# Kernel tuning notes

Measured on AMD Instinct MI355X. Metric: run time of the kernel, lower is better.

The kernel has to match this reference:

```python
import jax, jax.numpy as jnp
import numpy as np

N, M, D = 2048, 100000, 128
K = 5


def setup_inputs() -> dict:
    key = jax.random.key(0)
    k1, k2 = jax.random.split(key)
    features = jax.random.normal(k1, (N, D), dtype=jnp.float32)
    memory_bank = jax.random.normal(k2, (M, D), dtype=jnp.float32)
    # normalization buffers computed during fit(); use plausible scalars
    min_val = jnp.zeros((), dtype=jnp.float32)
    max_val = jnp.ones((), dtype=jnp.float32)
    return {
        "features": features,
        "memory_bank": memory_bank,
        "min_val": min_val,
        "max_val": max_val,
        "n_neighbors": K,
    }


def reference(features, memory_bank, min_val, max_val, n_neighbors):
    x2 = jnp.sum(features * features, axis=1, keepdims=True)        # (N,1)
    y2 = jnp.sum(memory_bank * memory_bank, axis=1)[None, :]        # (1,M)
    d2 = x2 + y2 - 2.0 * (features @ memory_bank.T)                 # (N,M)
    dist = jnp.sqrt(jnp.maximum(d2, 0.0))
    # k smallest distances per query (topk largest=False)
    neg_knn, _ = jax.lax.top_k(-dist, n_neighbors)                  # (N,K)
    knn = -neg_knn
    # min-max normalization with fitted stats
    knn = (knn - min_val) / (max_val - min_val)
    return knn.mean(axis=1)                                         # (N,)
```

## Files before the change

### kernel.cpp

```cpp
#include <hip/hip_runtime.h>
#include <stdint.h>

#define N_Q 2048
#define M_B 100000
#define D_DIM 128
#define KNN 5
#define SLABS_TOTAL 1563
#define M_PAD (SLABS_TOTAL * 64)
#define CHUNKS 64
#define SPC 25
#define CLS 16
#define FTOT (CHUNKS * CLS)
#define ROWBLOCKS 16
#define TROWS 128
#define BIGF 3.0e38f
#define NEGF -3.0e38f


typedef __attribute__((ext_vector_type(8))) short short8;
typedef __attribute__((ext_vector_type(4))) unsigned short ushort4v;
typedef __attribute__((ext_vector_type(8))) unsigned short ushort8v;
typedef __attribute__((ext_vector_type(4))) float f32x4;

static __device__ __forceinline__ unsigned short f2bf(float f) {
  unsigned int u = __builtin_bit_cast(unsigned int, f);
  u = (u + 0x7FFFu + ((u >> 16) & 1u)) >> 16;
  return (unsigned short)u;
}

static __device__ __forceinline__ void gload_lds16(const void* g, void* l) {
  __builtin_amdgcn_global_load_lds((const __attribute__((address_space(1))) unsigned int*)g,
                                   (__attribute__((address_space(3))) unsigned int*)l, 16, 0, 0);
}
static __device__ __forceinline__ void gload_lds4(const void* g, void* l) {
  __builtin_amdgcn_global_load_lds((const __attribute__((address_space(1))) unsigned int*)g,
                                   (__attribute__((address_space(3))) unsigned int*)l, 4, 0, 0);
}

#define DPPADD(v, ctrl)                                                              \
  do {                                                                               \
    int _t = __builtin_amdgcn_update_dpp(0, __builtin_bit_cast(int, (v)), (ctrl),    \
                                         0xf, 0xf, false);                           \
    (v) = (v) + __builtin_bit_cast(float, _t);                                       \
  } while (0)

__global__ __launch_bounds__(256) void k_prep(const float* __restrict__ Y,
                                              unsigned short* __restrict__ ybf,
                                              float* __restrict__ ny2) {
  const int s = blockIdx.x;
  const int t = threadIdx.x;
  __shared__ __align__(16) unsigned short tile[8192];
  __shared__ float redy[64 * 33];
#pragma unroll
  for (int i = 0; i < 8; ++i) {
    const int u = i * 256 + t;
    const int rowl = u >> 5;
    const int q = u & 31;
    const int rowg = s * 64 + rowl;
    const int rowc = (rowg < M_B) ? rowg : (M_B - 1);
    const float4 v = ((const float4*)Y)[(size_t)rowc * 32 + q];
    redy[rowl * 33 + q] = v.x * v.x + v.y * v.y + v.z * v.z + v.w * v.w;
    ushort4v o;
    o[0] = f2bf(v.x); o[1] = f2bf(v.y); o[2] = f2bf(v.z); o[3] = f2bf(v.w);
    *(ushort4v*)(tile + (size_t)(((q >> 1) * 64 + rowl) * 8 + (q & 1) * 4)) = o;
  }
  __syncthreads();
  {
    const int rowl = t >> 2;
    const int k = t & 3;
    float ss = 0.f;
#pragma unroll
    for (int j = 0; j < 8; ++j) ss += redy[rowl * 33 + k * 8 + j];
    DPPADD(ss, 0xB1);
    DPPADD(ss, 0x4E);
    const int rowg = s * 64 + rowl;
    if ((t & 3) == 0) ny2[(size_t)s * 64 + rowl] = (rowg < M_B) ? (-0.5f * ss) : NEGF;
  }
#pragma unroll
  for (int i = 0; i < 4; ++i) {
    const int u = i * 256 + t;
    *(ushort8v*)(ybf + ((size_t)s * 1024 + u) * 8) = *(const ushort8v*)(tile + u * 8);
  }
}

__global__ __launch_bounds__(256, 4) void k_main(const float* __restrict__ X,
                                                 const unsigned short* __restrict__ ybf,
                                                 const float* __restrict__ ny2,
                                                 float* __restrict__ rsm) {
  __shared__ __align__(16) char smem[39168];
  unsigned short* ys = (unsigned short*)smem;
  float* ny2s = (float*)(smem + 32768);

  const int bid = blockIdx.x;
  const int chunk = bid % CHUNKS;
  const int rowblock = bid / CHUNKS;
  const int row0 = rowblock * TROWS;

  const int cs0 = chunk * SPC;
  int nslab = SLABS_TOTAL - cs0;
  if (nslab > SPC) nslab = SPC;
  if (nslab < 0) nslab = 0;

  const int t = threadIdx.x;
  const int wave = t >> 6;
  const int lane = t & 63;
  const int lm = lane & 15;
  const int lq = lane >> 4;

  short8 afrag[2][4];
#pragma unroll
  for (int rt = 0; rt < 2; ++rt)
#pragma unroll
    for (int ks = 0; ks < 4; ++ks) {
      const float* xr = X + (size_t)(row0 + wave * 32 + rt * 16 + lm) * D_DIM + ks * 32 + lq * 8;
      const float4 a = *(const float4*)xr;
      const float4 b = *(const float4*)(xr + 4);
      short8 f;
      f[0] = (short)f2bf(a.x); f[1] = (short)f2bf(a.y);
      f[2] = (short)f2bf(a.z); f[3] = (short)f2bf(a.w);
      f[4] = (short)f2bf(b.x); f[5] = (short)f2bf(b.y);
      f[6] = (short)f2bf(b.z); f[7] = (short)f2bf(b.w);
      afrag[rt][ks] = f;
    }

  for (int j = wave; j < nslab; j += 4)
    gload_lds4(ny2 + (size_t)(cs0 + j) * 64 + lane, ny2s + (size_t)j * 64);
  __syncthreads();

  float prmax[2][4];
#pragma unroll
  for (int rt = 0; rt < 2; ++rt)
#pragma unroll
    for (int rr = 0; rr < 4; ++rr) prmax[rt][rr] = NEGF;

  if (nslab > 0) {
    const unsigned short* src = ybf + (size_t)cs0 * 8192;
#pragma unroll
    for (int i = 0; i < 4; ++i) {
      const int ub = i * 256 + wave * 64;
      gload_lds16(src + (size_t)(ub + lane) * 8, ys + (size_t)ub * 8);
    }
  }

  for (int s = 0; s < nslab; ++s) {
    unsigned short* yb = ys + (size_t)(s & 1) * 8192;
    if (s + 1 < nslab) {
      const unsigned short* src = ybf + (size_t)(cs0 + s + 1) * 8192;
      unsigned short* dst = ys + (size_t)((s + 1) & 1) * 8192;
#pragma unroll
      for (int i = 0; i < 4; ++i) {
        const int ub = i * 256 + wave * 64;
        gload_lds16(src + (size_t)(ub + lane) * 8, dst + (size_t)ub * 8);
      }
      asm volatile("s_waitcnt vmcnt(4)" ::: "memory");
    } else {
      asm volatile("s_waitcnt vmcnt(0)" ::: "memory");
    }
    __builtin_amdgcn_s_barrier();

    float y2c[4];
#pragma unroll
    for (int ct = 0; ct < 4; ++ct) y2c[ct] = ny2s[s * 64 + ct * 16 + lm];

    f32x4 acc[2][4];
#pragma unroll
    for (int rt = 0; rt < 2; ++rt)
#pragma unroll
      for (int ct = 0; ct < 4; ++ct)
#pragma unroll
        for (int rr = 0; rr < 4; ++rr) acc[rt][ct][rr] = y2c[ct];

    __builtin_amdgcn_s_setprio(1);
#pragma unroll
    for (int ct = 0; ct < 4; ++ct) {
      short8 bfr[4];
#pragma unroll
      for (int ks = 0; ks < 4; ++ks)
        bfr[ks] = *(const short8*)(yb + (size_t)(((ks * 4 + lq) * 64 + ct * 16 + lm)) * 8);
#pragma unroll
      for (int rt = 0; rt < 2; ++rt)
#pragma unroll
        for (int ks = 0; ks < 4; ++ks)
          acc[rt][ct] = __builtin_amdgcn_mfma_f32_16x16x32_bf16(afrag[rt][ks], bfr[ks],
                                                                acc[rt][ct], 0, 0, 0);
    }
    __builtin_amdgcn_s_setprio(0);

#pragma unroll
    for (int rt = 0; rt < 2; ++rt)
#pragma unroll
      for (int rr = 0; rr < 4; ++rr) {
        const float cm = fmaxf(fmaxf(fmaxf(acc[rt][0][rr], acc[rt][1][rr]),
                                     acc[rt][2][rr]), acc[rt][3][rr]);
        prmax[rt][rr] = fmaxf(prmax[rt][rr], cm);
      }

    __builtin_amdgcn_s_barrier();
  }

#pragma unroll
  for (int rt = 0; rt < 2; ++rt)
#pragma unroll
    for (int rr = 0; rr < 4; ++rr) {
      const int lrow = wave * 32 + rt * 16 + lq * 4 + rr;
      rsm[(size_t)(row0 + lrow) * FTOT + chunk * CLS + lm] = prmax[rt][rr];
    }
}

__global__ __launch_bounds__(256) void k_scan(const float* __restrict__ rsm,
                                              const float* __restrict__ X,
                                              const float* __restrict__ minp,
                                              const float* __restrict__ maxp,
                                              float* __restrict__ out) {
  const int wave = threadIdx.x >> 6;
  const int lane = threadIdx.x & 63;
  const int row = blockIdx.x * 4 + wave;
  const float* rp = rsm + (size_t)row * FTOT;

  float x2;
  {
    const float a = X[(size_t)row * D_DIM + lane];
    const float b = X[(size_t)row * D_DIM + 64 + lane];
    x2 = a * a + b * b;
#pragma unroll
    for (int off = 1; off < 64; off <<= 1) x2 += __shfl_xor(x2, off);
  }

  float t0 = NEGF, t1 = NEGF, t2 = NEGF, t3 = NEGF, t4 = NEGF;
  for (int i = lane; i < FTOT; i += 64) {
    const float v = rp[i];
    if (v > t4) {
      float m = v;
      float n3 = fminf(t3, m); m = fmaxf(t3, m);
      float n2 = fminf(t2, m); m = fmaxf(t2, m);
      float n1 = fminf(t1, m); m = fmaxf(t1, m);
      float n0 = fminf(t0, m); m = fmaxf(t0, m);
      t0 = m; t1 = n0; t2 = n1; t3 = n2; t4 = n3;
    }
  }

  int k = 0;
  float sum = 0.f;
#pragma unroll
  for (int r = 0; r < KNN; ++r) {
    float head = (k == 0) ? t0 : (k == 1) ? t1 : (k == 2) ? t2 : (k == 3) ? t3
               : (k == 4) ? t4 : NEGF;
    float m = head;
#pragma unroll
    for (int off = 1; off < 64; off <<= 1) m = fmaxf(m, __shfl_xor(m, off));
    const unsigned long long mask = __ballot(head == m);
    const int first = __ffsll(mask) - 1;
    if (lane == first) ++k;
    sum += sqrtf(fmaxf(x2 - 2.f * m, 0.f));
  }
  if (lane == 0) {
    const float mn = minp[0], mx = maxp[0];
    out[row] = (sum * (1.0f / KNN) - mn) / (mx - mn);
  }
}

extern "C" void kernel_launch(void* const* d_in, const int* in_sizes, int n_in,
                              void* d_out, int out_size, void* d_ws, size_t ws_size,
                              hipStream_t stream) {
  const float* X = (const float*)d_in[0];
  const float* Y = (const float*)d_in[1];
  const float* minp = (const float*)d_in[2];
  const float* maxp = (const float*)d_in[3];
  float* out = (float*)d_out;

  char* ws = (char*)d_ws;
  size_t off = 0;
  unsigned short* ybf = (unsigned short*)(ws + off); off += (size_t)M_PAD * D_DIM * 2;
  float* ny2 = (float*)(ws + off);                   off += (size_t)M_PAD * 4;
  float* rsm = (float*)(ws + off);                   off += (size_t)N_Q * FTOT * 4;

  k_prep<<<dim3(SLABS_TOTAL), dim3(256), 0, stream>>>(Y, ybf, ny2);
  k_main<<<dim3(ROWBLOCKS * CHUNKS), dim3(256), 0, stream>>>(X, ybf, ny2, rsm);
  k_scan<<<dim3(N_Q / 4), dim3(256), 0, stream>>>(rsm, X, minp, maxp, out);
}
```

Baseline: 146.7 us.

## Switch main GEMM to 32x32x16 MFMA with 256-row tiles per block

Replaces the 16x16x32 bf16 MFMA tiling with 32x32x16 MFMA and doubles rows per block from 128 to 256, so each wave covers 64 query rows. The LDS layout of the memory-bank slab is read with a new per-lane offset, and per-row maxima are merged across lane halves with a shuffle before being written. The aim is to reuse each B fragment across more rows, halving how often the bank is streamed from global memory, and to lower MFMA issue overhead. In exchange it uses more registers (occupancy hint drops from 4 to 2 blocks per CU), launches half as many blocks, and removes the setprio hints.

```diff
diff --git a/kernel.cpp b/kernel.cpp
--- a/kernel.cpp
+++ b/kernel.cpp
@@ -11,8 +11,8 @@
 #define SPC 25
 #define CLS 16
 #define FTOT (CHUNKS * CLS)
-#define ROWBLOCKS 16
-#define TROWS 128
+#define ROWBLOCKS 8
+#define TROWS 256
 #define BIGF 3.0e38f
 #define NEGF -3.0e38f
 
@@ -20,7 +20,7 @@
 typedef __attribute__((ext_vector_type(8))) short short8;
 typedef __attribute__((ext_vector_type(4))) unsigned short ushort4v;
 typedef __attribute__((ext_vector_type(8))) unsigned short ushort8v;
-typedef __attribute__((ext_vector_type(4))) float f32x4;
+typedef __attribute__((ext_vector_type(16))) float f32x16;
 
 static __device__ __forceinline__ unsigned short f2bf(float f) {
   unsigned int u = __builtin_bit_cast(unsigned int, f);
@@ -83,7 +83,7 @@
   }
 }
 
-__global__ __launch_bounds__(256, 4) void k_main(const float* __restrict__ X,
+__global__ __launch_bounds__(256, 2) void k_main(const float* __restrict__ X,
                                                  const unsigned short* __restrict__ ybf,
                                                  const float* __restrict__ ny2,
                                                  float* __restrict__ rsm) {
@@ -104,15 +104,15 @@
   const int t = threadIdx.x;
   const int wave = t >> 6;
   const int lane = t & 63;
-  const int lm = lane & 15;
-  const int lq = lane >> 4;
-
-  short8 afrag[2][4];
+  const int l31 = lane & 31;
+  const int lq5 = lane >> 5;
+
+  short8 afrag[2][8];
 #pragma unroll
   for (int rt = 0; rt < 2; ++rt)
 #pragma unroll
-    for (int ks = 0; ks < 4; ++ks) {
-      const float* xr = X + (size_t)(row0 + wave * 32 + rt * 16 + lm) * D_DIM + ks * 32 + lq * 8;
+    for (int ks = 0; ks < 8; ++ks) {
+      const float* xr = X + (size_t)(row0 + wave * 64 + rt * 32 + l31) * D_DIM + ks * 16 + lq5 * 8;
       const float4 a = *(const float4*)xr;
       const float4 b = *(const float4*)(xr + 4);
       short8 f;
@@ -127,11 +127,13 @@
     gload_lds4(ny2 + (size_t)(cs0 + j) * 64 + lane, ny2s + (size_t)j * 64);
   __syncthreads();
 
-  float prmax[2][4];
+  float prmax[2][16];
 #pragma unroll
   for (int rt = 0; rt < 2; ++rt)
 #pragma unroll
-    for (int rr = 0; rr < 4; ++rr) prmax[rt][rr] = NEGF;
+    for (int r = 0; r < 16; ++r) prmax[rt][r] = NEGF;
+
+  const int blane = lq5 * 512 + l31 * 8;
 
   if (nslab > 0) {
     const unsigned short* src = ybf + (size_t)cs0 * 8192;
@@ -143,10 +145,10 @@
   }
 
   for (int s = 0; s < nslab; ++s) {
-    unsigned short* yb = ys + (size_t)(s & 1) * 8192;
+    const unsigned short* yb = ys + (size_t)((s & 1) * 8192) + blane;
     if (s + 1 < nslab) {
       const unsigned short* src = ybf + (size_t)(cs0 + s + 1) * 8192;
-      unsigned short* dst = ys + (size_t)((s + 1) & 1) * 8192;
+      unsigned short* dst = ys + (size_t)(((s + 1) & 1) * 8192);
 #pragma unroll
       for (int i = 0; i < 4; ++i) {
         const int ub = i * 256 + wave * 64;
@@ -158,52 +160,53 @@
     }
     __builtin_amdgcn_s_barrier();
 
-    float y2c[4];
-#pragma unroll
-    for (int ct = 0; ct < 4; ++ct) y2c[ct] = ny2s[s * 64 + ct * 16 + lm];
-
-    f32x4 acc[2][4];
+    const float y2c0 = ny2s[s * 64 + l31];
+    const float y2c1 = ny2s[s * 64 + 32 + l31];
+
+    f32x16 acc[2][2];
 #pragma unroll
     for (int rt = 0; rt < 2; ++rt)
 #pragma unroll
-      for (int ct = 0; ct < 4; ++ct)
-#pragma unroll
-        for (int rr = 0; rr < 4; ++rr) acc[rt][ct][rr] = y2c[ct];
-
-    __builtin_amdgcn_s_setprio(1);
-#pragma unroll
-    for (int ct = 0; ct < 4; ++ct) {
-      short8 bfr[4];
-#pragma unroll
-      for (int ks = 0; ks < 4; ++ks)
-        bfr[ks] = *(const short8*)(yb + (size_t)(((ks * 4 + lq) * 64 + ct * 16 + lm)) * 8);
+      for (int r = 0; r < 16; ++r) {
+        acc[rt][0][r] = y2c0;
+        acc[rt][1][r] = y2c1;
+      }
+
+    short8 bfr[2][8];
+#pragma unroll
+    for (int ct = 0; ct < 2; ++ct)
+#pragma unroll
+      for (int ks = 0; ks < 8; ++ks)
+        bfr[ct][ks] = *(const short8*)(yb + ks * 1024 + ct * 256);
+
+#pragma unroll
+    for (int ct = 0; ct < 2; ++ct)
 #pragma unroll
       for (int rt = 0; rt < 2; ++rt)
 #pragma unroll
-        for (int ks = 0; ks < 4; ++ks)
-          acc[rt][ct] = __builtin_amdgcn_mfma_f32_16x16x32_bf16(afrag[rt][ks], bfr[ks],
+        for (int ks = 0; ks < 8; ++ks)
+          acc[rt][ct] = __builtin_amdgcn_mfma_f32_32x32x16_bf16(afrag[rt][ks], bfr[ct][ks],
                                                                 acc[rt][ct], 0, 0, 0);
-    }
-    __builtin_amdgcn_s_setprio(0);
 
 #pragma unroll
     for (int rt = 0; rt < 2; ++rt)
 #pragma unroll
-      for (int rr = 0; rr < 4; ++rr) {
-        const float cm = fmaxf(fmaxf(fmaxf(acc[rt][0][rr], acc[rt][1][rr]),
-                                     acc[rt][2][rr]), acc[rt][3][rr]);
-        prmax[rt][rr] = fmaxf(prmax[rt][rr], cm);
+      for (int r = 0; r < 16; ++r)
+        prmax[rt][r] = fmaxf(prmax[rt][r], fmaxf(acc[rt][0][r], acc[rt][1][r]));
+
+    __builtin_amdgcn_s_barrier();
+  }
+
+#pragma unroll
+  for (int rt = 0; rt < 2; ++rt)
+#pragma unroll
+    for (int r = 0; r < 16; ++r) {
+      float v = prmax[rt][r];
+      v = fmaxf(v, __shfl_xor(v, 16));
+      if ((lane & 16) == 0) {
+        const int lrow = wave * 64 + rt * 32 + (r & 3) + 8 * (r >> 2) + 4 * lq5;
+        rsm[(size_t)(row0 + lrow) * FTOT + chunk * CLS + (lane & 15)] = v;
       }
-
-    __builtin_amdgcn_s_barrier();
-  }
-
-#pragma unroll
-  for (int rt = 0; rt < 2; ++rt)
-#pragma unroll
-    for (int rr = 0; rr < 4; ++rr) {
-      const int lrow = wave * 32 + rt * 16 + lq * 4 + rr;
-      rsm[(size_t)(row0 + lrow) * FTOT + chunk * CLS + lm] = prmax[rt][rr];
     }
 }
 
```

Measured after the change: 152.0 us. 3.6% more time.
